# Kernel tuning notes

Measured on AMD Instinct MI355X. Metric: run time of the kernel, lower is better.

Reference implementation:

```python
import jax, jax.numpy as jnp
import numpy as np

C, H, V, K, B, T = 1024, 256, 10000, 32, 8, 256
K1K = 2 * K + 1


def setup_inputs() -> dict:
    key = jax.random.key(0)
    ks = jax.random.split(key, 12)
    s = 0.05
    n = lambda k, shp: jax.random.normal(k, shp, dtype=jnp.float32) * s
    z = lambda shp: jnp.zeros(shp, dtype=jnp.float32)
    return {
        'text': jax.random.randint(ks[0], (B, T), 0, V, dtype=jnp.int32),
        'start_emb': n(ks[1], (H,)),
        'start_lin_W': n(ks[2], (H, H)), 'start_lin_b': z((H,)),
        'start_res_W1': n(ks[3], (2, H, H)), 'start_res_b1': z((2, H)),
        'start_res_W2': n(ks[4], (2, H, H)), 'start_res_b2': z((2, H)),
        'state_emb': n(ks[5], (C, H)),
        'next_state_emb': n(ks[6], (C, H)),
        'preterminal_emb': n(ks[7], (C, H)),
        'term_res_W1': n(ks[8], (2, H, H)), 'term_res_b1': z((2, H)),
        'term_res_W2': n(ks[9], (2, H, H)), 'term_res_b2': z((2, H)),
        'terminal_emb': n(ks[10], (V, H)),
        'col_banded_transition': n(ks[11], (C, K1K)),
    }


def _res(x, W1, b1, W2, b2):
    # ResLayer: x + ReLU(Linear(ReLU(Linear(x))))
    h = jax.nn.relu(x @ W1.T + b1)
    h = jax.nn.relu(h @ W2.T + b2)
    return x + h


def _band_to_dense(band):
    # BandedMatrix(band[None], K, K, fill=0).to_dense(): dense[i, i+d] = band[i, d+K] for |d|<=K
    offs = jnp.arange(-K, K + 1)                  # (K1K,)
    rows = jnp.arange(C)
    cols = rows[:, None] + offs[None, :]          # (C, K1K)
    valid = (cols >= 0) & (cols < C)
    vals = jnp.where(valid, band, 0.0)
    return jnp.zeros((C, C), band.dtype).at[rows[:, None], jnp.clip(cols, 0, C - 1)].add(vals)


def reference(text, start_emb, start_lin_W, start_lin_b,
              start_res_W1, start_res_b1, start_res_W2, start_res_b2,
              state_emb, next_state_emb, preterminal_emb,
              term_res_W1, term_res_b1, term_res_W2, term_res_b2,
              terminal_emb, col_banded_transition):
    # start(): MLP(start_emb) @ next_state_emb.T (tie_start), log_softmax -> (C,)
    fx = start_emb @ start_lin_W.T + start_lin_b
    for i in range(2):
        fx = _res(fx, start_res_W1[i], start_res_b1[i], start_res_W2[i], start_res_b2[i])
    start = jax.nn.log_softmax(fx @ next_state_emb.T)

    # transition(): dense logits + banded logits (band_method='product'), row log_softmax -> (C, C)
    logits = state_emb @ next_state_emb.T
    trans = jax.nn.log_softmax(logits + _band_to_dense(col_banded_transition), axis=-1)

    # emission(): terminal_mlp(preterminal_emb) @ terminal_emb.T, log_softmax -> (C, V)
    ft = preterminal_emb
    for i in range(2):
        ft = _res(ft, term_res_W1[i], term_res_b1[i], term_res_W2[i], term_res_b2[i])
    emit_T = jax.nn.log_softmax(ft @ terminal_emb.T, axis=-1).T  # (V, C)

    # HMM forward algorithm over time (log semiring)
    alpha = start[None, :] + emit_T[text[:, 0]]  # (B, C)

    def step(alpha, toks):
        # alpha_next[b, j] = logsumexp_i(alpha[b, i] + trans[i, j]) + emit[j, tok_b]
        a = jax.nn.logsumexp(alpha[:, :, None] + trans[None], axis=1) + emit_T[toks]
        return a, None

    alpha, _ = jax.lax.scan(step, alpha, text[:, 1:].T)
    return jax.nn.logsumexp(alpha, axis=-1)  # (B,) log-evidence
```

## Files before the change

kernel.cpp:

```cpp
#include <hip/hip_runtime.h>

constexpr int C = 1024, H = 256, V = 10000, K = 32, B = 8, T = 256, K1K = 65;
constexpr int DB = 32;
constexpr int GSCAN = B * DB;
constexpr float LV = 9.210340371976184f;
constexpr unsigned SENT = 0x80000000u;

#define DEV static __device__ __forceinline__

typedef float f4 __attribute__((ext_vector_type(4)));

DEV void gstore(float* p, float v) {
  __hip_atomic_store((unsigned*)p, __float_as_uint(v), __ATOMIC_RELAXED, __HIP_MEMORY_SCOPE_AGENT);
}
DEV float gload(const float* p) {
  return __uint_as_float(__hip_atomic_load((unsigned*)p, __ATOMIC_RELAXED, __HIP_MEMORY_SCOPE_AGENT));
}

__global__ void __launch_bounds__(256) k_pre(
    const float* __restrict__ semb, const float* __restrict__ linW, const float* __restrict__ linb,
    const float* __restrict__ srW1, const float* __restrict__ srb1,
    const float* __restrict__ srW2, const float* __restrict__ srb2,
    const float* __restrict__ nse, const float* __restrict__ se,
    const float* __restrict__ pre, const float* __restrict__ trW1, const float* __restrict__ trb1,
    const float* __restrict__ trW2, const float* __restrict__ trb2,
    const float* __restrict__ band,
    float* __restrict__ pay, float* __restrict__ startv,
    float* __restrict__ ft, float* __restrict__ PT) {
  __shared__ float smem[2048];
  const int bid = blockIdx.x, tid = threadIdx.x;

  if (bid < 16) {
    unsigned* p = (unsigned*)pay;
    #pragma unroll
    for (int k = 0; k < 8; ++k) p[bid * 2048 + k * 256 + tid] = SENT;
    return;
  }

  if (bid == 16) {
    float* sa = smem;
    float* fx = smem + 256;
    float* hh = smem + 512;
    float* sl = smem + 768;
    float* red = smem + 1792;
    sa[tid] = semb[tid];
    __syncthreads();
    float acc = linb[tid];
    for (int h = 0; h < H; ++h) acc += sa[h] * linW[tid * H + h];
    fx[tid] = acc;
    __syncthreads();
    for (int l = 0; l < 2; ++l) {
      float a1 = srb1[l * H + tid];
      const float* w1 = srW1 + (size_t)l * H * H + (size_t)tid * H;
      for (int h = 0; h < H; ++h) a1 += fx[h] * w1[h];
      hh[tid] = fmaxf(a1, 0.f);
      __syncthreads();
      float a2 = srb2[l * H + tid];
      const float* w2 = srW2 + (size_t)l * H * H + (size_t)tid * H;
      for (int h = 0; h < H; ++h) a2 += hh[h] * w2[h];
      __syncthreads();
      fx[tid] += fmaxf(a2, 0.f);
      __syncthreads();
    }
    for (int q = 0; q < 4; ++q) {
      int c = q * 256 + tid;
      const float* nr = nse + (size_t)c * H;
      float s = 0.f;
      for (int h = 0; h < H; ++h) s += fx[h] * nr[h];
      sl[c] = s;
    }
    __syncthreads();
    float m = -__builtin_inff();
    for (int q = 0; q < 4; ++q) m = fmaxf(m, sl[q * 256 + tid]);
    red[tid] = m; __syncthreads();
    for (int off = 128; off > 0; off >>= 1) { if (tid < off) red[tid] = fmaxf(red[tid], red[tid + off]); __syncthreads(); }
    m = red[0]; __syncthreads();
    float s = 0.f;
    for (int q = 0; q < 4; ++q) s += __expf(sl[q * 256 + tid] - m);
    red[tid] = s; __syncthreads();
    for (int off = 128; off > 0; off >>= 1) { if (tid < off) red[tid] += red[tid + off]; __syncthreads(); }
    float lse = m + __logf(red[0]);
    for (int q = 0; q < 4; ++q) { int c = q * 256 + tid; startv[c] = sl[c] - lse; }
    return;
  }

  if (bid < 273) {
    float (*x)[H] = (float(*)[H])smem;
    float (*hh)[H] = (float(*)[H])(smem + 1024);
    int r0 = (bid - 17) * 4;
    for (int r = 0; r < 4; ++r) x[r][tid] = pre[(size_t)(r0 + r) * H + tid];
    __syncthreads();
    for (int l = 0; l < 2; ++l) {
      {
        const f4* w1 = (const f4*)(trW1 + (size_t)l * H * H + (size_t)tid * H);
        f4 p0 = {0.f, 0.f, 0.f, 0.f}, p1 = p0, p2 = p0, p3 = p0;
        #pragma unroll 8
        for (int h4 = 0; h4 < H / 4; ++h4) {
          f4 w = w1[h4];
          p0 += w * *(const f4*)&x[0][h4 * 4];
          p1 += w * *(const f4*)&x[1][h4 * 4];
          p2 += w * *(const f4*)&x[2][h4 * 4];
          p3 += w * *(const f4*)&x[3][h4 * 4];
        }
        float bb = trb1[l * H + tid];
        hh[0][tid] = fmaxf(p0.x + p0.y + p0.z + p0.w + bb, 0.f);
        hh[1][tid] = fmaxf(p1.x + p1.y + p1.z + p1.w + bb, 0.f);
        hh[2][tid] = fmaxf(p2.x + p2.y + p2.z + p2.w + bb, 0.f);
        hh[3][tid] = fmaxf(p3.x + p3.y + p3.z + p3.w + bb, 0.f);
      }
      __syncthreads();
      {
        const f4* w2 = (const f4*)(trW2 + (size_t)l * H * H + (size_t)tid * H);
        f4 q0 = {0.f, 0.f, 0.f, 0.f}, q1 = q0, q2 = q0, q3 = q0;
        #pragma unroll 8
        for (int h4 = 0; h4 < H / 4; ++h4) {
          f4 w = w2[h4];
          q0 += w * *(const f4*)&hh[0][h4 * 4];
          q1 += w * *(const f4*)&hh[1][h4 * 4];
          q2 += w * *(const f4*)&hh[2][h4 * 4];
          q3 += w * *(const f4*)&hh[3][h4 * 4];
        }
        float bb = trb2[l * H + tid];
        __syncthreads();
        x[0][tid] += fmaxf(q0.x + q0.y + q0.z + q0.w + bb, 0.f);
        x[1][tid] += fmaxf(q1.x + q1.y + q1.z + q1.w + bb, 0.f);
        x[2][tid] += fmaxf(q2.x + q2.y + q2.z + q2.w + bb, 0.f);
        x[3][tid] += fmaxf(q3.x + q3.y + q3.z + q3.w + bb, 0.f);
      }
      __syncthreads();
    }
    for (int r = 0; r < 4; ++r) ft[(size_t)(r0 + r) * H + tid] = x[r][tid];
    return;
  }

  {
    float* sv = smem;
    float* sl = smem + 256;
    float* rr = smem + 1280;
    int i = bid - 273;
    sv[tid] = se[(size_t)i * H + tid];
    __syncthreads();
    #pragma unroll 1
    for (int jq = 0; jq < 4; ++jq) {
      int j = jq * 256 + tid;
      const float4* nr = (const float4*)(nse + (size_t)j * H);
      float acc = 0.f;
      #pragma unroll 8
      for (int h4 = 0; h4 < H / 4; ++h4) {
        float4 nv = nr[h4];
        float4 s4 = *(const float4*)&sv[h4 * 4];
        acc += s4.x * nv.x + s4.y * nv.y + s4.z * nv.z + s4.w * nv.w;
      }
      sl[j] = acc;
    }
    __syncthreads();
    if (tid < K1K) {
      int col = i + tid - K;
      if (col >= 0 && col < C) sl[col] += band[(size_t)i * K1K + tid];
    }
    __syncthreads();
    float m = -__builtin_inff();
    for (int q = 0; q < 4; ++q) m = fmaxf(m, sl[q * 256 + tid]);
    rr[tid] = m; __syncthreads();
    for (int off = 128; off > 0; off >>= 1) { if (tid < off) rr[tid] = fmaxf(rr[tid], rr[tid + off]); __syncthreads(); }
    m = rr[0]; __syncthreads();
    float e[4]; float s = 0.f;
    for (int q = 0; q < 4; ++q) { e[q] = __expf(sl[q * 256 + tid] - m); s += e[q]; }
    rr[tid] = s; __syncthreads();
    for (int off = 128; off > 0; off >>= 1) { if (tid < off) rr[tid] += rr[tid + off]; __syncthreads(); }
    float inv = 1.f / rr[0];
    for (int q = 0; q < 4; ++q) {
      int j = q * 256 + tid;
      PT[(size_t)j * C + i] = e[q] * inv;
    }
  }
}

__global__ void __launch_bounds__(256) k_denom_part(
    const float* __restrict__ ft, const float* __restrict__ term, float* __restrict__ dpart) {
  constexpr int TJ = 16, VC = V / 8;
  __shared__ float shs[TJ * 4];
  int tid = threadIdx.x, lane = tid & 63, w = tid >> 6;
  int jg = blockIdx.x >> 3, vc = blockIdx.x & 7;
  const float4* fb = (const float4*)(ft + (size_t)jg * TJ * H);
  float rs[TJ];
  #pragma unroll
  for (int r = 0; r < TJ; ++r) rs[r] = 0.f;
  int v0 = vc * VC;
  for (int v = v0 + tid; v < v0 + VC; v += 256) {
    const float4* tr = (const float4*)(term + (size_t)v * H);
    float acc[TJ];
    #pragma unroll
    for (int r = 0; r < TJ; ++r) acc[r] = 0.f;
    for (int h4 = 0; h4 < H / 4; ++h4) {
      float4 tv = tr[h4];
      #pragma unroll
      for (int r = 0; r < TJ; ++r) {
        float4 f = fb[r * (H / 4) + h4];
        acc[r] += tv.x * f.x + tv.y * f.y + tv.z * f.z + tv.w * f.w;
      }
    }
    #pragma unroll
    for (int r = 0; r < TJ; ++r) rs[r] += __expf(acc[r]);
  }
  #pragma unroll
  for (int r = 0; r < TJ; ++r) {
    float s = rs[r];
    #pragma unroll
    for (int off = 32; off > 0; off >>= 1) s += __shfl_xor(s, off);
    if (lane == 0) shs[r * 4 + w] = s;
  }
  __syncthreads();
  if (tid < TJ) {
    float s = shs[tid * 4] + shs[tid * 4 + 1] + shs[tid * 4 + 2] + shs[tid * 4 + 3];
    dpart[(jg * TJ + tid) * 8 + vc] = s;
  }
}

__global__ void __launch_bounds__(256) k_eemit(
    const int* __restrict__ text, const float* __restrict__ ft,
    const float* __restrict__ dpart, const float* __restrict__ term,
    float* __restrict__ eem) {
  int tid = threadIdx.x;
  int n0 = blockIdx.x * 8;
  const float4* trow[8];
  #pragma unroll
  for (int r = 0; r < 8; ++r) {
    int n = n0 + r;
    int tok = text[(n & 7) * T + (n >> 3)];
    trow[r] = (const float4*)(term + (size_t)tok * H);
  }
  for (int q = 0; q < 4; ++q) {
    int j = q * 256 + tid;
    const float4* fr = (const float4*)(ft + (size_t)j * H);
    float acc[8];
    #pragma unroll
    for (int r = 0; r < 8; ++r) acc[r] = 0.f;
    for (int h4 = 0; h4 < H / 4; ++h4) {
      float4 f = fr[h4];
      #pragma unroll
      for (int r = 0; r < 8; ++r) {
        float4 tv = trow[r][h4];
        acc[r] += f.x * tv.x + f.y * tv.y + f.z * tv.z + f.w * tv.w;
      }
    }
    f4 d0 = *(const f4*)&dpart[j * 8];
    f4 d1 = *(const f4*)&dpart[j * 8 + 4];
    float dj = __logf(d0.x + d0.y + d0.z + d0.w + d1.x + d1.y + d1.z + d1.w);
    #pragma unroll
    for (int r = 0; r < 8; ++r) eem[(size_t)(n0 + r) * C + j] = __expf(acc[r] - dj + LV);
  }
}

#define PLOAD(k) f4 p##k = prow[k];
#define PDOT(k) { f4 x = *(const f4*)&us[ubo + (k) * 4]; \
  acc += p##k.x * x.x + p##k.y * x.y + p##k.z * x.z + p##k.w * x.w; }
#define PPIN8(a,b,c,d,e,f,g,h) asm volatile("" : "+v"(p##a), "+v"(p##b), "+v"(p##c), \
  "+v"(p##d), "+v"(p##e), "+v"(p##f), "+v"(p##g), "+v"(p##h));

__global__ void __launch_bounds__(256, 1) k_scan(
    const float* __restrict__ PT, const float* __restrict__ eem,
    const float* __restrict__ startv, float* __restrict__ pay,
    float* __restrict__ umax, float* __restrict__ out) {
  __shared__ __align__(16) float us[8 * 132];
  __shared__ float wv[32];
  __shared__ float fred[256];
  const int tid = threadIdx.x, bid = blockIdx.x;
  const int b = bid & 7, blk = bid >> 3;
  const int jloc = tid >> 3, s = tid & 7;
  const int myj = blk * 32 + jloc;
  const bool owner = (s == 0);

  const f4* prow = (const f4*)(PT + (size_t)myj * C + s * 128);
  PLOAD(0) PLOAD(1) PLOAD(2) PLOAD(3) PLOAD(4) PLOAD(5) PLOAD(6) PLOAD(7)
  PLOAD(8) PLOAD(9) PLOAD(10) PLOAD(11) PLOAD(12) PLOAD(13) PLOAD(14) PLOAD(15)
  PLOAD(16) PLOAD(17) PLOAD(18) PLOAD(19) PLOAD(20) PLOAD(21) PLOAD(22) PLOAD(23)
  PLOAD(24) PLOAD(25) PLOAD(26) PLOAD(27) PLOAD(28) PLOAD(29) PLOAD(30) PLOAD(31)

  float Sacc = 0.f;

  if (owner) {
    float u0 = __expf(startv[myj]) * eem[(size_t)b * C + myj];
    gstore(&pay[(size_t)b * C + myj], u0);
  }
  float em = owner ? eem[((size_t)B + b) * C + myj] : 0.f;

  const int pi = tid * 4;
  const int ph = (pi >> 7) * 132 + (pi & 127);
  const int ubo = s * 132;

  for (int t = 1; t < T; ++t) {
    {
      const float* src = pay + (size_t)((t - 1) & 3) * (B * C) + (size_t)b * C + pi;
      f4 r;
      for (;;) {
        asm volatile("global_load_dwordx4 %0, %1, off sc0 sc1\n\ts_waitcnt vmcnt(0)"
                     : "=v"(r) : "v"(src) : "memory");
        unsigned bits = __float_as_uint(r.x) | __float_as_uint(r.y) |
                        __float_as_uint(r.z) | __float_as_uint(r.w);
        if (!(bits & 0x80000000u)) break;
        __builtin_amdgcn_s_sleep(1);
      }
      *(f4*)&us[ph] = r;
    }
    __syncthreads();

    float imt = 1.f;
    if (owner && (t & 7) == 1 && t > 1) {
      float m = gload(&umax[((t - 1) >> 3) * 8 + b]);
      imt = 1.f / m;
      Sacc += __logf(m);
    }

    PPIN8(0,1,2,3,4,5,6,7) PPIN8(8,9,10,11,12,13,14,15)
    PPIN8(16,17,18,19,20,21,22,23) PPIN8(24,25,26,27,28,29,30,31)

    float acc = 0.f;
    PDOT(0) PDOT(1) PDOT(2) PDOT(3) PDOT(4) PDOT(5) PDOT(6) PDOT(7)
    PDOT(8) PDOT(9) PDOT(10) PDOT(11) PDOT(12) PDOT(13) PDOT(14) PDOT(15)
    PDOT(16) PDOT(17) PDOT(18) PDOT(19) PDOT(20) PDOT(21) PDOT(22) PDOT(23)
    PDOT(24) PDOT(25) PDOT(26) PDOT(27) PDOT(28) PDOT(29) PDOT(30) PDOT(31)
    acc += __shfl_xor(acc, 1);
    acc += __shfl_xor(acc, 2);
    acc += __shfl_xor(acc, 4);

    float val = 0.f;
    if (owner) val = acc * imt * em;

    if (blk == 0 && (t & 7) == 0) {
      if (owner) wv[jloc] = val;
      __syncthreads();
      if (tid == 0) {
        float m = wv[0];
        #pragma unroll
        for (int j2 = 1; j2 < 32; ++j2) m = fmaxf(m, wv[j2]);
        gstore(&umax[(t >> 3) * 8 + b], m);
        asm volatile("s_waitcnt vmcnt(0)" ::: "memory");
      }
    }

    if (owner) gstore(&pay[(size_t)(t & 3) * (B * C) + (size_t)b * C + myj], val);

    if (tid < 8) {
      float* dst = pay + (size_t)((t + 1) & 3) * (B * C) + (size_t)b * C + blk * 32 + tid * 4;
      f4 sn;
      sn.x = sn.y = sn.z = sn.w = __uint_as_float(SENT);
      asm volatile("global_store_dwordx4 %0, %1, off sc0 sc1" :: "v"(dst), "v"(sn) : "memory");
    }
    if (owner && t + 1 < T) em = eem[((size_t)(t + 1) * B + b) * C + myj];
  }

  if (blk == 0) {
    {
      const float* src = pay + (size_t)((T - 1) & 3) * (B * C) + (size_t)b * C + pi;
      f4 r;
      for (;;) {
        asm volatile("global_load_dwordx4 %0, %1, off sc0 sc1\n\ts_waitcnt vmcnt(0)"
                     : "=v"(r) : "v"(src) : "memory");
        unsigned bits = __float_as_uint(r.x) | __float_as_uint(r.y) |
                        __float_as_uint(r.z) | __float_as_uint(r.w);
        if (!(bits & 0x80000000u)) break;
        __builtin_amdgcn_s_sleep(1);
      }
      fred[tid] = r.x + r.y + r.z + r.w;
    }
    __syncthreads();
    for (int off = 128; off > 0; off >>= 1) {
      if (tid < off) fred[tid] += fred[tid + off];
      __syncthreads();
    }
    if (tid == 0) out[b] = -(float)T * LV + Sacc + __logf(fred[0]);
  }
}

extern "C" void kernel_launch(void* const* d_in, const int* in_sizes, int n_in,
                              void* d_out, int out_size, void* d_ws, size_t ws_size,
                              hipStream_t stream) {
  const int*   text  = (const int*)  d_in[0];
  const float* semb  = (const float*)d_in[1];
  const float* slinW = (const float*)d_in[2];
  const float* slinb = (const float*)d_in[3];
  const float* srW1  = (const float*)d_in[4];
  const float* srb1  = (const float*)d_in[5];
  const float* srW2  = (const float*)d_in[6];
  const float* srb2  = (const float*)d_in[7];
  const float* stemb = (const float*)d_in[8];
  const float* nse   = (const float*)d_in[9];
  const float* pre   = (const float*)d_in[10];
  const float* trW1  = (const float*)d_in[11];
  const float* trb1  = (const float*)d_in[12];
  const float* trW2  = (const float*)d_in[13];
  const float* trb2  = (const float*)d_in[14];
  const float* term  = (const float*)d_in[15];
  const float* band  = (const float*)d_in[16];

  float* ws     = (float*)d_ws;
  float* PT     = ws;
  float* eem    = PT + (size_t)C * C;
  float* pay    = eem + (size_t)T * B * C;
  float* ftb    = pay + 4 * B * C;
  float* startv = ftb + (size_t)C * H;
  float* dpart  = startv + C;
  float* umax   = dpart + C * 8;

  k_pre<<<1297, 256, 0, stream>>>(semb, slinW, slinb, srW1, srb1, srW2, srb2,
                                  nse, stemb, pre, trW1, trb1, trW2, trb2, band,
                                  pay, startv, ftb, PT);
  k_denom_part<<<(C / 16) * 8, 256, 0, stream>>>(ftb, term, dpart);
  k_eemit<<<(T * B) / 8, 256, 0, stream>>>(text, ftb, dpart, term, eem);
  k_scan<<<GSCAN, 256, 0, stream>>>(PT, eem, startv, pay, umax, (float*)d_out);
}
```

Baseline: 913.9 us.

## Batch transition rows per block, unroll vocab loop, asm-load PT and reorder scan step

The transition-row blocks in k_pre now handle four rows each, so every nse row load serves four dot products and the grid shrinks accordingly. k_denom_part replaces its strided vocabulary loop with four interleaved row streams plus a tail, to raise memory-level parallelism and reuse of the ft loads. In k_scan the PT register preload becomes inline-asm loads, the dot product uses a vector accumulator, and the sentinel store and next-emission load move before the dot product so they overlap it. The cost is more register pressure and bypassing the compiler's load scheduling, and the asm loads carry no explicit wait before first use.

```diff
diff --git a/kernel.cpp b/kernel.cpp
--- a/kernel.cpp
+++ b/kernel.cpp
@@ -27,7 +27,7 @@
     const float* __restrict__ band,
     float* __restrict__ pay, float* __restrict__ startv,
     float* __restrict__ ft, float* __restrict__ PT) {
-  __shared__ float smem[2048];
+  __shared__ float smem[5376];
   const int bid = blockIdx.x, tid = threadIdx.x;
 
   if (bid < 16) {
@@ -135,43 +135,58 @@
 
   {
     float* sv = smem;
-    float* sl = smem + 256;
-    float* rr = smem + 1280;
-    int i = bid - 273;
-    sv[tid] = se[(size_t)i * H + tid];
+    float* sl = smem + 1024;
+    float* rr = smem + 5120;
+    int i0 = (bid - 273) * 4;
+    for (int r = 0; r < 4; ++r) sv[r * 256 + tid] = se[(size_t)(i0 + r) * H + tid];
     __syncthreads();
     #pragma unroll 1
     for (int jq = 0; jq < 4; ++jq) {
       int j = jq * 256 + tid;
-      const float4* nr = (const float4*)(nse + (size_t)j * H);
-      float acc = 0.f;
+      const f4* nr = (const f4*)(nse + (size_t)j * H);
+      float a0 = 0.f, a1 = 0.f, a2 = 0.f, a3 = 0.f;
       #pragma unroll 8
       for (int h4 = 0; h4 < H / 4; ++h4) {
-        float4 nv = nr[h4];
-        float4 s4 = *(const float4*)&sv[h4 * 4];
-        acc += s4.x * nv.x + s4.y * nv.y + s4.z * nv.z + s4.w * nv.w;
-      }
-      sl[j] = acc;
+        f4 nv = nr[h4];
+        f4 s0 = *(const f4*)&sv[0 * 256 + h4 * 4];
+        f4 s1 = *(const f4*)&sv[1 * 256 + h4 * 4];
+        f4 s2 = *(const f4*)&sv[2 * 256 + h4 * 4];
+        f4 s3 = *(const f4*)&sv[3 * 256 + h4 * 4];
+        a0 += nv.x * s0.x + nv.y * s0.y + nv.z * s0.z + nv.w * s0.w;
+        a1 += nv.x * s1.x + nv.y * s1.y + nv.z * s1.z + nv.w * s1.w;
+        a2 += nv.x * s2.x + nv.y * s2.y + nv.z * s2.z + nv.w * s2.w;
+        a3 += nv.x * s3.x + nv.y * s3.y + nv.z * s3.z + nv.w * s3.w;
+      }
+      sl[0 * 1024 + j] = a0; sl[1 * 1024 + j] = a1;
+      sl[2 * 1024 + j] = a2; sl[3 * 1024 + j] = a3;
     }
     __syncthreads();
     if (tid < K1K) {
-      int col = i + tid - K;
-      if (col >= 0 && col < C) sl[col] += band[(size_t)i * K1K + tid];
-    }
-    __syncthreads();
-    float m = -__builtin_inff();
-    for (int q = 0; q < 4; ++q) m = fmaxf(m, sl[q * 256 + tid]);
-    rr[tid] = m; __syncthreads();
-    for (int off = 128; off > 0; off >>= 1) { if (tid < off) rr[tid] = fmaxf(rr[tid], rr[tid + off]); __syncthreads(); }
-    m = rr[0]; __syncthreads();
-    float e[4]; float s = 0.f;
-    for (int q = 0; q < 4; ++q) { e[q] = __expf(sl[q * 256 + tid] - m); s += e[q]; }
-    rr[tid] = s; __syncthreads();
-    for (int off = 128; off > 0; off >>= 1) { if (tid < off) rr[tid] += rr[tid + off]; __syncthreads(); }
-    float inv = 1.f / rr[0];
-    for (int q = 0; q < 4; ++q) {
-      int j = q * 256 + tid;
-      PT[(size_t)j * C + i] = e[q] * inv;
+      #pragma unroll
+      for (int r = 0; r < 4; ++r) {
+        int col = i0 + r + tid - K;
+        if (col >= 0 && col < C) sl[r * 1024 + col] += band[(size_t)(i0 + r) * K1K + tid];
+      }
+    }
+    __syncthreads();
+    #pragma unroll 1
+    for (int r = 0; r < 4; ++r) {
+      float* slr = sl + r * 1024;
+      float m = -__builtin_inff();
+      for (int q = 0; q < 4; ++q) m = fmaxf(m, slr[q * 256 + tid]);
+      rr[tid] = m; __syncthreads();
+      for (int off = 128; off > 0; off >>= 1) { if (tid < off) rr[tid] = fmaxf(rr[tid], rr[tid + off]); __syncthreads(); }
+      m = rr[0]; __syncthreads();
+      float e[4]; float s = 0.f;
+      for (int q = 0; q < 4; ++q) { e[q] = __expf(slr[q * 256 + tid] - m); s += e[q]; }
+      rr[tid] = s; __syncthreads();
+      for (int off = 128; off > 0; off >>= 1) { if (tid < off) rr[tid] += rr[tid + off]; __syncthreads(); }
+      float inv = 1.f / rr[0];
+      for (int q = 0; q < 4; ++q) {
+        int j = q * 256 + tid;
+        PT[(size_t)j * C + i0 + r] = e[q] * inv;
+      }
+      __syncthreads();
     }
   }
 }
@@ -182,26 +197,49 @@
   __shared__ float shs[TJ * 4];
   int tid = threadIdx.x, lane = tid & 63, w = tid >> 6;
   int jg = blockIdx.x >> 3, vc = blockIdx.x & 7;
-  const float4* fb = (const float4*)(ft + (size_t)jg * TJ * H);
+  const f4* fb = (const f4*)(ft + (size_t)jg * TJ * H);
   float rs[TJ];
   #pragma unroll
   for (int r = 0; r < TJ; ++r) rs[r] = 0.f;
   int v0 = vc * VC;
-  for (int v = v0 + tid; v < v0 + VC; v += 256) {
-    const float4* tr = (const float4*)(term + (size_t)v * H);
-    float acc[TJ];
-    #pragma unroll
-    for (int r = 0; r < TJ; ++r) acc[r] = 0.f;
+  {
+    const f4* t0 = (const f4*)(term + (size_t)(v0 + tid) * H);
+    const f4* t1 = t0 + 256 * (H / 4);
+    const f4* t2 = t1 + 256 * (H / 4);
+    const f4* t3 = t2 + 256 * (H / 4);
+    float a0[TJ], a1[TJ], a2[TJ], a3[TJ];
+    #pragma unroll
+    for (int r = 0; r < TJ; ++r) { a0[r] = 0.f; a1[r] = 0.f; a2[r] = 0.f; a3[r] = 0.f; }
     for (int h4 = 0; h4 < H / 4; ++h4) {
-      float4 tv = tr[h4];
+      f4 w0 = t0[h4], w1 = t1[h4], w2 = t2[h4], w3 = t3[h4];
       #pragma unroll
       for (int r = 0; r < TJ; ++r) {
-        float4 f = fb[r * (H / 4) + h4];
-        acc[r] += tv.x * f.x + tv.y * f.y + tv.z * f.z + tv.w * f.w;
-      }
-    }
-    #pragma unroll
-    for (int r = 0; r < TJ; ++r) rs[r] += __expf(acc[r]);
+        f4 f = fb[r * (H / 4) + h4];
+        a0[r] += f.x * w0.x + f.y * w0.y + f.z * w0.z + f.w * w0.w;
+        a1[r] += f.x * w1.x + f.y * w1.y + f.z * w1.z + f.w * w1.w;
+        a2[r] += f.x * w2.x + f.y * w2.y + f.z * w2.z + f.w * w2.w;
+        a3[r] += f.x * w3.x + f.y * w3.y + f.z * w3.z + f.w * w3.w;
+      }
+    }
+    #pragma unroll
+    for (int r = 0; r < TJ; ++r)
+      rs[r] += __expf(a0[r]) + __expf(a1[r]) + __expf(a2[r]) + __expf(a3[r]);
+  }
+  if (tid < VC - 1024) {
+    const f4* tt = (const f4*)(term + (size_t)(v0 + 1024 + tid) * H);
+    float at[TJ];
+    #pragma unroll
+    for (int r = 0; r < TJ; ++r) at[r] = 0.f;
+    for (int h4 = 0; h4 < H / 4; ++h4) {
+      f4 wt = tt[h4];
+      #pragma unroll
+      for (int r = 0; r < TJ; ++r) {
+        f4 f = fb[r * (H / 4) + h4];
+        at[r] += f.x * wt.x + f.y * wt.y + f.z * wt.z + f.w * wt.w;
+      }
+    }
+    #pragma unroll
+    for (int r = 0; r < TJ; ++r) rs[r] += __expf(at[r]);
   }
   #pragma unroll
   for (int r = 0; r < TJ; ++r) {
@@ -252,11 +290,9 @@
   }
 }
 
-#define PLOAD(k) f4 p##k = prow[k];
-#define PDOT(k) { f4 x = *(const f4*)&us[ubo + (k) * 4]; \
-  acc += p##k.x * x.x + p##k.y * x.y + p##k.z * x.z + p##k.w * x.w; }
-#define PPIN8(a,b,c,d,e,f,g,h) asm volatile("" : "+v"(p##a), "+v"(p##b), "+v"(p##c), \
-  "+v"(p##d), "+v"(p##e), "+v"(p##f), "+v"(p##g), "+v"(p##h));
+#define PLOADA(k, ofs) \
+  asm volatile("global_load_dwordx4 %0, %1, off offset:" #ofs : "=v"(p##k) : "v"(pb));
+#define PDOT(k) { f4 x = *(const f4*)&us[ubo + (k) * 4]; facc += p##k * x; }
 
 __global__ void __launch_bounds__(256, 1) k_scan(
     const float* __restrict__ PT, const float* __restrict__ eem,
@@ -271,11 +307,17 @@
   const int myj = blk * 32 + jloc;
   const bool owner = (s == 0);
 
-  const f4* prow = (const f4*)(PT + (size_t)myj * C + s * 128);
-  PLOAD(0) PLOAD(1) PLOAD(2) PLOAD(3) PLOAD(4) PLOAD(5) PLOAD(6) PLOAD(7)
-  PLOAD(8) PLOAD(9) PLOAD(10) PLOAD(11) PLOAD(12) PLOAD(13) PLOAD(14) PLOAD(15)
-  PLOAD(16) PLOAD(17) PLOAD(18) PLOAD(19) PLOAD(20) PLOAD(21) PLOAD(22) PLOAD(23)
-  PLOAD(24) PLOAD(25) PLOAD(26) PLOAD(27) PLOAD(28) PLOAD(29) PLOAD(30) PLOAD(31)
+  const float* pb = PT + (size_t)myj * C + s * 128;
+  f4 p0, p1, p2, p3, p4, p5, p6, p7, p8, p9, p10, p11, p12, p13, p14, p15;
+  f4 p16, p17, p18, p19, p20, p21, p22, p23, p24, p25, p26, p27, p28, p29, p30, p31;
+  PLOADA(0, 0)    PLOADA(1, 16)   PLOADA(2, 32)   PLOADA(3, 48)
+  PLOADA(4, 64)   PLOADA(5, 80)   PLOADA(6, 96)   PLOADA(7, 112)
+  PLOADA(8, 128)  PLOADA(9, 144)  PLOADA(10, 160) PLOADA(11, 176)
+  PLOADA(12, 192) PLOADA(13, 208) PLOADA(14, 224) PLOADA(15, 240)
+  PLOADA(16, 256) PLOADA(17, 272) PLOADA(18, 288) PLOADA(19, 304)
+  PLOADA(20, 320) PLOADA(21, 336) PLOADA(22, 352) PLOADA(23, 368)
+  PLOADA(24, 384) PLOADA(25, 400) PLOADA(26, 416) PLOADA(27, 432)
+  PLOADA(28, 448) PLOADA(29, 464) PLOADA(30, 480) PLOADA(31, 496)
 
   float Sacc = 0.f;
 
@@ -305,6 +347,15 @@
     }
     __syncthreads();
 
+    if (tid < 8) {
+      float* dst = pay + (size_t)((t + 1) & 3) * (B * C) + (size_t)b * C + blk * 32 + tid * 4;
+      f4 sn;
+      sn.x = sn.y = sn.z = sn.w = __uint_as_float(SENT);
+      asm volatile("global_store_dwordx4 %0, %1, off sc0 sc1" :: "v"(dst), "v"(sn) : "memory");
+    }
+    float em_next = em;
+    if (owner && t + 1 < T) em_next = eem[((size_t)(t + 1) * B + b) * C + myj];
+
     float imt = 1.f;
     if (owner && (t & 7) == 1 && t > 1) {
       float m = gload(&umax[((t - 1) >> 3) * 8 + b]);
@@ -312,14 +363,12 @@
       Sacc += __logf(m);
     }
 
-    PPIN8(0,1,2,3,4,5,6,7) PPIN8(8,9,10,11,12,13,14,15)
-    PPIN8(16,17,18,19,20,21,22,23) PPIN8(24,25,26,27,28,29,30,31)
-
-    float acc = 0.f;
+    f4 facc = {0.f, 0.f, 0.f, 0.f};
     PDOT(0) PDOT(1) PDOT(2) PDOT(3) PDOT(4) PDOT(5) PDOT(6) PDOT(7)
     PDOT(8) PDOT(9) PDOT(10) PDOT(11) PDOT(12) PDOT(13) PDOT(14) PDOT(15)
     PDOT(16) PDOT(17) PDOT(18) PDOT(19) PDOT(20) PDOT(21) PDOT(22) PDOT(23)
     PDOT(24) PDOT(25) PDOT(26) PDOT(27) PDOT(28) PDOT(29) PDOT(30) PDOT(31)
+    float acc = facc.x + facc.y + facc.z + facc.w;
     acc += __shfl_xor(acc, 1);
     acc += __shfl_xor(acc, 2);
     acc += __shfl_xor(acc, 4);
@@ -340,14 +389,7 @@
     }
 
     if (owner) gstore(&pay[(size_t)(t & 3) * (B * C) + (size_t)b * C + myj], val);
-
-    if (tid < 8) {
-      float* dst = pay + (size_t)((t + 1) & 3) * (B * C) + (size_t)b * C + blk * 32 + tid * 4;
-      f4 sn;
-      sn.x = sn.y = sn.z = sn.w = __uint_as_float(SENT);
-      asm volatile("global_store_dwordx4 %0, %1, off sc0 sc1" :: "v"(dst), "v"(sn) : "memory");
-    }
-    if (owner && t + 1 < T) em = eem[((size_t)(t + 1) * B + b) * C + myj];
+    em = em_next;
   }
 
   if (blk == 0) {
@@ -403,9 +445,9 @@
   float* dpart  = startv + C;
   float* umax   = dpart + C * 8;
 
-  k_pre<<<1297, 256, 0, stream>>>(semb, slinW, slinb, srW1, srb1, srW2, srb2,
-                                  nse, stemb, pre, trW1, trb1, trW2, trb2, band,
-                                  pay, startv, ftb, PT);
+  k_pre<<<529, 256, 0, stream>>>(semb, slinW, slinb, srW1, srb1, srW2, srb2,
+                                 nse, stemb, pre, trW1, trb1, trW2, trb2, band,
+                                 pay, startv, ftb, PT);
   k_denom_part<<<(C / 16) * 8, 256, 0, stream>>>(ftb, term, dpart);
   k_eemit<<<(T * B) / 8, 256, 0, stream>>>(text, ftb, dpart, term, eem);
   k_scan<<<GSCAN, 256, 0, stream>>>(PT, eem, startv, pay, umax, (float*)d_out);
```

Result: faster. 881.1 us (-3.6%).
